# Kernel optimization log

Hardware: AMD Instinct MI355X
Metric: run time of the kernel (lower is better)

## Reference

```python
import jax, jax.numpy as jnp
import numpy as np

N_GRAPHS = 64

def setup_inputs() -> dict:
    key = jax.random.key(0)
    ks = jax.random.split(key, 8)
    N, E, H = 50000, 600000, 128
    x = jax.random.normal(ks[0], (N, 2), dtype=jnp.float32)
    edge_index = jax.random.randint(ks[1], (2, E), 0, N, dtype=jnp.int64)
    batch = jnp.sort(jax.random.randint(ks[2], (N,), 0, N_GRAPHS, dtype=jnp.int64))
    s = 0.1  # keep tanh out of saturation
    return {
        'x': x,
        'edge_index': edge_index,
        'batch': batch,
        'W1': jax.random.normal(ks[3], (2, H), dtype=jnp.float32) * s,
        'b1': jnp.zeros((H,), jnp.float32),
        'W2': jax.random.normal(ks[4], (H, H), dtype=jnp.float32) * s,
        'b2': jnp.zeros((H,), jnp.float32),
        'W3': jax.random.normal(ks[5], (H, H), dtype=jnp.float32) * s,
        'b3': jnp.zeros((H,), jnp.float32),
        'Wo': jax.random.normal(ks[6], (2 * H, 41), dtype=jnp.float32) * s,
        'bo': jnp.zeros((41,), jnp.float32),
    }

def reference(x, edge_index, batch, W1, b1, W2, b2, W3, b3, Wo, bo):
    N = x.shape[0]
    src, dst = edge_index[0], edge_index[1]
    # GCN symmetric normalization with self loops: deg = in-degree + 1
    ones_e = jnp.ones(src.shape[0], dtype=x.dtype)
    deg = jax.ops.segment_sum(ones_e, dst, num_segments=N) + 1.0
    dinv = jax.lax.rsqrt(deg)                       # [N]
    edge_norm = (dinv[src] * dinv[dst])[:, None]    # [E,1]
    self_norm = (dinv * dinv)[:, None]              # [N,1]

    def gcn(h, W, b):
        h = h @ W                                   # [N,H] transform first
        agg = jax.ops.segment_sum(h[src] * edge_norm, dst, num_segments=N)
        return agg + h * self_norm + b

    h = jnp.tanh(gcn(x, W1, b1))
    h = jnp.tanh(gcn(h, W2, b2))
    h = jnp.tanh(gcn(h, W3, b3))

    # global max pool + global mean pool over graphs
    cnt = jax.ops.segment_sum(jnp.ones(N, dtype=h.dtype), batch, num_segments=N_GRAPHS)
    mx = jax.ops.segment_max(h, batch, num_segments=N_GRAPHS)
    mx = jnp.where(cnt[:, None] > 0, mx, 0.0)
    mean = jax.ops.segment_sum(h, batch, num_segments=N_GRAPHS) / jnp.maximum(cnt, 1.0)[:, None]
    pooled = jnp.concatenate([mx, mean], axis=1)    # [G, 2H]
    return jnp.tanh(pooled @ Wo + bo)               # [G, 41]
```

## Files before the change

### kernel.cpp

```cpp
#include <hip/hip_runtime.h>
#include <math.h>

#define NGRAPH 64
#define POOL_CHUNKS 32
#define SCAN_BLK 1024

typedef short short8 __attribute__((ext_vector_type(8)));
typedef float floatx4 __attribute__((ext_vector_type(4)));

__device__ inline unsigned pack_bf16x2(float a, float b) {
    unsigned ua = __float_as_uint(a);
    unsigned ub = __float_as_uint(b);
    ua = (ua + 0x7fffu + ((ua >> 16) & 1u)) >> 16;
    ub = (ub + 0x7fffu + ((ub >> 16) & 1u)) >> 16;
    return ua | (ub << 16);
}
__device__ inline unsigned short bf16_1(float a) {
    unsigned ua = __float_as_uint(a);
    return (unsigned short)((ua + 0x7fffu + ((ua >> 16) & 1u)) >> 16);
}
__device__ inline float bf16lo(unsigned u) { return __uint_as_float(u << 16); }
__device__ inline float bf16hi(unsigned u) { return __uint_as_float(u & 0xffff0000u); }


__global__ void pack_count(const int* __restrict__ dst, int E, int* __restrict__ cnt,
                           const float* __restrict__ W2, const float* __restrict__ W3,
                           unsigned* __restrict__ Wt2, unsigned* __restrict__ Wt3) {
    if (blockIdx.x < 32) {
        int b = blockIdx.x;
        const float* W = (b < 16) ? W2 : W3;
        unsigned* Wt = (b < 16) ? Wt2 : Wt3;
        b &= 15;
        int bk = b & 3, bn = b >> 2;
        __shared__ float s[32][33];
        int tx = threadIdx.x & 31, ty = threadIdx.x >> 5;
#pragma unroll
        for (int r = 0; r < 4; ++r)
            s[r * 8 + ty][tx] = W[(bk * 32 + r * 8 + ty) * 128 + bn * 32 + tx];
        __syncthreads();
        int t16 = threadIdx.x & 15, tn = threadIdx.x >> 4;
#pragma unroll
        for (int pass = 0; pass < 2; ++pass) {
            int nl = pass * 16 + tn;
            unsigned pk = pack_bf16x2(s[2 * t16][nl], s[2 * t16 + 1][nl]);
            Wt[(bn * 32 + nl) * 64 + bk * 16 + t16] = pk;
        }
    } else {
        int e = (blockIdx.x - 32) * blockDim.x + threadIdx.x;
        if (e < E) atomicAdd(&cnt[dst[e]], 1);
    }
}


__global__ __launch_bounds__(SCAN_BLK) void scan_phase1(const int* __restrict__ cnt,
                                                        const float* __restrict__ x,
                                                        int* __restrict__ row_ptr,
                                                        int* __restrict__ bsum,
                                                        float* __restrict__ dinv,
                                                        float2* __restrict__ y, int N) {
    __shared__ int sm[SCAN_BLK];
    int i = blockIdx.x * SCAN_BLK + threadIdx.x;
    int v = (i < N) ? cnt[i] : 0;
    if (i < N) {
        float dv = rsqrtf((float)v + 1.0f);
        dinv[i] = dv;
        float2 xv = ((const float2*)x)[i];
        y[i] = make_float2(xv.x * dv, xv.y * dv);
    }
    sm[threadIdx.x] = v;
    __syncthreads();
    for (int off = 1; off < SCAN_BLK; off <<= 1) {
        int t = (threadIdx.x >= (unsigned)off) ? sm[threadIdx.x - off] : 0;
        __syncthreads();
        sm[threadIdx.x] += t;
        __syncthreads();
    }
    if (i < N) row_ptr[i] = sm[threadIdx.x] - v;
    if (threadIdx.x == SCAN_BLK - 1) bsum[blockIdx.x] = sm[SCAN_BLK - 1];
}

__global__ __launch_bounds__(SCAN_BLK) void scan_phase2(int* __restrict__ bsum, int nb,
                                                        const int* __restrict__ batch, int N,
                                                        int* __restrict__ goff) {
    if (threadIdx.x <= NGRAPH) {
        int g = threadIdx.x;
        int lo = 0, hi = N;
        while (lo < hi) {
            int mid = (lo + hi) >> 1;
            if (batch[mid] < g) lo = mid + 1; else hi = mid;
        }
        goff[g] = lo;
    }
    __shared__ int sm[SCAN_BLK];
    int v = (threadIdx.x < (unsigned)nb) ? bsum[threadIdx.x] : 0;
    sm[threadIdx.x] = v;
    __syncthreads();
    for (int off = 1; off < SCAN_BLK; off <<= 1) {
        int t = (threadIdx.x >= (unsigned)off) ? sm[threadIdx.x - off] : 0;
        __syncthreads();
        sm[threadIdx.x] += t;
        __syncthreads();
    }
    if (threadIdx.x < (unsigned)nb) bsum[threadIdx.x] = sm[threadIdx.x] - v;
}

__global__ __launch_bounds__(SCAN_BLK) void scan_phase3(int* __restrict__ row_ptr,
                                                        const int* __restrict__ bsum,
                                                        int N, int E) {
    int i = blockIdx.x * SCAN_BLK + threadIdx.x;
    if (i < N) row_ptr[i] += bsum[blockIdx.x];
    if (i == 0) row_ptr[N] = E;
}

__global__ void fill_kernel(const int* __restrict__ src, const int* __restrict__ dst, int E,
                            const int* __restrict__ row_ptr, int* __restrict__ cnt,
                            int* __restrict__ col) {
    int e = blockIdx.x * blockDim.x + threadIdx.x;
    if (e < E) {
        int d = dst[e];
        int p = row_ptr[d] + atomicSub(&cnt[d], 1) - 1;
        col[p] = src[e];
    }
}


__global__ __launch_bounds__(256) void agg_x_t1(const float2* __restrict__ y,
                                                const int* __restrict__ row_ptr,
                                                const int* __restrict__ col,
                                                const float* __restrict__ dinv,
                                                const float* __restrict__ W1,
                                                const float* __restrict__ b1,
                                                unsigned short* __restrict__ h, int N) {
    __shared__ float4 sW[64];
    __shared__ float4 sb[32];
    __shared__ float2 zs[256];
    if (threadIdx.x < 64) sW[threadIdx.x] = ((const float4*)W1)[threadIdx.x];
    if (threadIdx.x < 32) sb[threadIdx.x] = ((const float4*)b1)[threadIdx.x];

    int v = blockIdx.x * 256 + threadIdx.x;
    float2 zv = make_float2(0.f, 0.f);
    if (v < N) {
        int s = row_ptr[v], e = row_ptr[v + 1];
        float2 a0 = y[v];
        float2 a1 = make_float2(0.f, 0.f);
        float2 a2 = make_float2(0.f, 0.f);
        float2 a3 = make_float2(0.f, 0.f);
        int j = s;
        for (; j + 4 <= e; j += 4) {
            int u0 = col[j], u1 = col[j + 1], u2 = col[j + 2], u3 = col[j + 3];
            float2 v0 = y[u0], v1 = y[u1], v2 = y[u2], v3 = y[u3];
            a0.x += v0.x; a0.y += v0.y;
            a1.x += v1.x; a1.y += v1.y;
            a2.x += v2.x; a2.y += v2.y;
            a3.x += v3.x; a3.y += v3.y;
        }
        for (; j < e; ++j) {
            float2 vv = y[col[j]];
            a0.x += vv.x; a0.y += vv.y;
        }
        float dv = dinv[v];
        zv = make_float2(dv * (a0.x + a1.x + a2.x + a3.x),
                         dv * (a0.y + a1.y + a2.y + a3.y));
    }
    zs[threadIdx.x] = zv;
    __syncthreads();

    int q = threadIdx.x & 31;
    int rsub = threadIdx.x >> 5;
    float4 w0 = sW[q];
    float4 w1 = sW[32 + q];
    float4 b = sb[q];
#pragma unroll 4
    for (int pass = 0; pass < 32; ++pass) {
        int local = pass * 8 + rsub;
        int row = blockIdx.x * 256 + local;
        if (row >= N) break;
        float2 z = zs[local];
        float ox = tanhf(fmaf(z.x, w0.x, fmaf(z.y, w1.x, b.x)));
        float oy = tanhf(fmaf(z.x, w0.y, fmaf(z.y, w1.y, b.y)));
        float oz = tanhf(fmaf(z.x, w0.z, fmaf(z.y, w1.z, b.z)));
        float ow = tanhf(fmaf(z.x, w0.w, fmaf(z.y, w1.w, b.w)));
        uint2 pk;
        pk.x = pack_bf16x2(ox, oy);
        pk.y = pack_bf16x2(oz, ow);
        ((uint2*)h)[(size_t)row * 32 + q] = pk;
    }
}


__global__ __launch_bounds__(256) void gemm_mfma(const unsigned short* __restrict__ A,
                                                 const unsigned* __restrict__ Wt,
                                                 const float* __restrict__ dinv,
                                                 unsigned short* __restrict__ t, int N) {
    __shared__ unsigned sW[128 * 68];
    const uint4* Wt4 = (const uint4*)Wt;
    for (int i = threadIdx.x; i < 2048; i += 256) {
        int n = i >> 4, c = i & 15;
        *(uint4*)&sW[n * 68 + c * 4] = Wt4[i];
    }
    __syncthreads();
    int w = threadIdx.x >> 6;
    int l = threadIdx.x & 63;
    int lm = l & 15;
    int q4 = l >> 4;
    int k8 = q4 * 8;

    floatx4 acc[2][8];
#pragma unroll
    for (int i = 0; i < 2; ++i)
#pragma unroll
        for (int j = 0; j < 8; ++j) acc[i][j] = (floatx4){0.f, 0.f, 0.f, 0.f};

    int rowbase = blockIdx.x * 128 + w * 32;
#pragma unroll
    for (int ks = 0; ks < 4; ++ks) {
        int k0 = ks * 32 + k8;
        short8 a[2];
#pragma unroll
        for (int mt = 0; mt < 2; ++mt) {
            int r = min(rowbase + mt * 16 + lm, N - 1);
            a[mt] = *(const short8*)(A + (size_t)r * 128 + k0);
        }
#pragma unroll
        for (int nt = 0; nt < 8; ++nt) {
            short8 b = *(const short8*)&sW[(nt * 16 + lm) * 68 + ks * 16 + q4 * 4];
#pragma unroll
            for (int mt = 0; mt < 2; ++mt)
                acc[mt][nt] = __builtin_amdgcn_mfma_f32_16x16x32_bf16(a[mt], b, acc[mt][nt], 0, 0, 0);
        }
    }

#pragma unroll
    for (int mt = 0; mt < 2; ++mt) {
#pragma unroll
        for (int reg = 0; reg < 4; ++reg) {
            int gr = rowbase + mt * 16 + q4 * 4 + reg;
            if (gr >= N) continue;
            float dv = dinv[gr];
#pragma unroll
            for (int nt = 0; nt < 8; ++nt) {
                int c = nt * 16 + lm;
                t[(size_t)gr * 128 + c] = bf16_1(acc[mt][nt][reg] * dv);
            }
        }
    }
}


__global__ __launch_bounds__(256) void agg_kernel(const unsigned short* __restrict__ t,
                                                  const int* __restrict__ row_ptr,
                                                  const int* __restrict__ col,
                                                  const float* __restrict__ dinv,
                                                  const float* __restrict__ bias,
                                                  unsigned short* __restrict__ out, int N) {
    int wave = threadIdx.x >> 6;
    int lane = threadIdx.x & 63;
    int i = lane >> 4;
    int q = lane & 15;
    int node = blockIdx.x * 4 + wave;
    if (node >= N) return;
    int s = row_ptr[node];
    int deg = row_ptr[node + 1] - s;
    const uint4* t4 = (const uint4*)t;

    float a0[8], a1[8];
#pragma unroll
    for (int k = 0; k < 8; ++k) { a0[k] = 0.f; a1[k] = 0.f; }
    if (i == 0) {
        uint4 v = t4[(size_t)node * 16 + q];
        a0[0] = bf16lo(v.x); a0[1] = bf16hi(v.x);
        a0[2] = bf16lo(v.y); a0[3] = bf16hi(v.y);
        a0[4] = bf16lo(v.z); a0[5] = bf16hi(v.z);
        a0[6] = bf16lo(v.w); a0[7] = bf16hi(v.w);
    }
    int j = 0;
    for (; j + 8 <= deg; j += 8) {
        int u0 = col[s + j + i];
        int u1 = col[s + j + 4 + i];
        uint4 v0 = t4[(size_t)u0 * 16 + q];
        uint4 v1 = t4[(size_t)u1 * 16 + q];
        a0[0] += bf16lo(v0.x); a0[1] += bf16hi(v0.x);
        a0[2] += bf16lo(v0.y); a0[3] += bf16hi(v0.y);
        a0[4] += bf16lo(v0.z); a0[5] += bf16hi(v0.z);
        a0[6] += bf16lo(v0.w); a0[7] += bf16hi(v0.w);
        a1[0] += bf16lo(v1.x); a1[1] += bf16hi(v1.x);
        a1[2] += bf16lo(v1.y); a1[3] += bf16hi(v1.y);
        a1[4] += bf16lo(v1.z); a1[5] += bf16hi(v1.z);
        a1[6] += bf16lo(v1.w); a1[7] += bf16hi(v1.w);
    }
    for (; j < deg; j += 4) {
        if (j + i < deg) {
            int u = col[s + j + i];
            uint4 v = t4[(size_t)u * 16 + q];
            a0[0] += bf16lo(v.x); a0[1] += bf16hi(v.x);
            a0[2] += bf16lo(v.y); a0[3] += bf16hi(v.y);
            a0[4] += bf16lo(v.z); a0[5] += bf16hi(v.z);
            a0[6] += bf16lo(v.w); a0[7] += bf16hi(v.w);
        }
    }
#pragma unroll
    for (int k = 0; k < 8; ++k) {
        float v = a0[k] + a1[k];
        v += __shfl_xor(v, 16, 64);
        v += __shfl_xor(v, 32, 64);
        a0[k] = v;
    }
    if (i == 0) {
        float dv = dinv[node];
        float4 b0 = ((const float4*)bias)[2 * q];
        float4 b1 = ((const float4*)bias)[2 * q + 1];
        uint4 pk;
        pk.x = pack_bf16x2(tanhf(fmaf(dv, a0[0], b0.x)), tanhf(fmaf(dv, a0[1], b0.y)));
        pk.y = pack_bf16x2(tanhf(fmaf(dv, a0[2], b0.z)), tanhf(fmaf(dv, a0[3], b0.w)));
        pk.z = pack_bf16x2(tanhf(fmaf(dv, a0[4], b1.x)), tanhf(fmaf(dv, a0[5], b1.y)));
        pk.w = pack_bf16x2(tanhf(fmaf(dv, a0[6], b1.z)), tanhf(fmaf(dv, a0[7], b1.w)));
        ((uint4*)out)[(size_t)node * 16 + q] = pk;
    }
}


__global__ __launch_bounds__(128) void pool_partial(const unsigned short* __restrict__ h,
                                                    const int* __restrict__ goff,
                                                    float* __restrict__ part) {
    int g = blockIdx.x;
    int c = blockIdx.y;
    int j = threadIdx.x;
    int s = goff[g], e = goff[g + 1];
    int cnt = e - s;
    int per = (cnt + POOL_CHUNKS - 1) / POOL_CHUNKS;
    int ps = s + c * per;
    int pe = min(ps + per, e);
    float mx = -3.402823466e+38f, sm = 0.f;
    for (int n = ps; n < pe; ++n) {
        float v = __uint_as_float(((unsigned)h[(size_t)n * 128 + j]) << 16);
        mx = fmaxf(mx, v);
        sm += v;
    }
    float* dst = part + ((size_t)g * POOL_CHUNKS + c) * 256;
    dst[j] = mx;
    dst[128 + j] = sm;
}

__global__ __launch_bounds__(128) void pool_final(const float* __restrict__ part,
                                                  const int* __restrict__ goff,
                                                  const float* __restrict__ Wo,
                                                  const float* __restrict__ bo,
                                                  float* __restrict__ out) {
    __shared__ float p[256];
    int g = blockIdx.x;
    int j = threadIdx.x;
    float mx = -3.402823466e+38f, sm = 0.f;
    const float* base = part + (size_t)g * POOL_CHUNKS * 256;
#pragma unroll 4
    for (int c = 0; c < POOL_CHUNKS; ++c) {
        mx = fmaxf(mx, base[c * 256 + j]);
        sm += base[c * 256 + 128 + j];
    }
    int cnt = goff[g + 1] - goff[g];
    p[j] = (cnt > 0) ? mx : 0.f;
    p[128 + j] = sm / fmaxf((float)cnt, 1.f);
    __syncthreads();
    if (j < 41) {
        float acc = bo[j];
        for (int k = 0; k < 256; ++k) acc = fmaf(p[k], Wo[k * 41 + j], acc);
        out[g * 41 + j] = tanhf(acc);
    }
}


extern "C" void kernel_launch(void* const* d_in, const int* in_sizes, int n_in,
                              void* d_out, int out_size, void* d_ws, size_t ws_size,
                              hipStream_t stream) {
    const float* x   = (const float*)d_in[0];
    const int*   ei  = (const int*)d_in[1];
    const int* batch = (const int*)d_in[2];
    const float* W1  = (const float*)d_in[3];
    const float* b1  = (const float*)d_in[4];
    const float* W2  = (const float*)d_in[5];
    const float* b2  = (const float*)d_in[6];
    const float* W3  = (const float*)d_in[7];
    const float* b3  = (const float*)d_in[8];
    const float* Wo  = (const float*)d_in[9];
    const float* bo  = (const float*)d_in[10];
    float* outp = (float*)d_out;

    int N = in_sizes[2];
    int E = in_sizes[1] / 2;
    const int* src = ei;
    const int* dst = ei + E;

    char* p = (char*)d_ws;
    auto alloc = [&](size_t bytes) -> char* {
        char* q = p;
        p += (bytes + 255) & ~(size_t)255;
        return q;
    };
    unsigned short* t   = (unsigned short*)alloc((size_t)N * 128 * 2);
    unsigned short* hb  = (unsigned short*)alloc((size_t)N * 128 * 2);
    unsigned short* h3b = (unsigned short*)alloc((size_t)N * 128 * 2);
    float* dinv   = (float*)alloc((size_t)N * 4);
    int*   cnt    = (int*)alloc((size_t)N * 4);
    int*   rowp   = (int*)alloc((size_t)(N + 1) * 4);
    int*   col    = (int*)alloc((size_t)E * 4);
    int*   goff   = (int*)alloc(65 * 4);
    float* part   = (float*)alloc((size_t)NGRAPH * POOL_CHUNKS * 256 * 4);
    float2* y     = (float2*)alloc((size_t)N * 8);
    unsigned* Wt2 = (unsigned*)alloc(128 * 64 * 4);
    unsigned* Wt3 = (unsigned*)alloc(128 * 64 * 4);
    int nscan = (N + SCAN_BLK - 1) / SCAN_BLK;
    int*   bsum   = (int*)alloc((size_t)nscan * 4);

    hipMemsetAsync(cnt, 0, (size_t)N * 4, stream);

    pack_count<<<32 + (E + 255) / 256, 256, 0, stream>>>(dst, E, cnt, W2, W3, Wt2, Wt3);
    scan_phase1<<<nscan, SCAN_BLK, 0, stream>>>(cnt, x, rowp, bsum, dinv, y, N);
    scan_phase2<<<1, SCAN_BLK, 0, stream>>>(bsum, nscan, batch, N, goff);
    scan_phase3<<<nscan, SCAN_BLK, 0, stream>>>(rowp, bsum, N, E);
    fill_kernel<<<(E + 255) / 256, 256, 0, stream>>>(src, dst, E, rowp, cnt, col);

    agg_x_t1<<<(N + 255) / 256, 256, 0, stream>>>(y, rowp, col, dinv, W1, b1, hb, N);
    gemm_mfma<<<(N + 127) / 128, 256, 0, stream>>>(hb, Wt2, dinv, t, N);
    agg_kernel<<<(N + 3) / 4, 256, 0, stream>>>(t, rowp, col, dinv, b2, hb, N);
    gemm_mfma<<<(N + 127) / 128, 256, 0, stream>>>(hb, Wt3, dinv, t, N);
    agg_kernel<<<(N + 3) / 4, 256, 0, stream>>>(t, rowp, col, dinv, b3, h3b, N);

    dim3 pgrid(NGRAPH, POOL_CHUNKS);
    pool_partial<<<pgrid, 128, 0, stream>>>(h3b, goff, part);
    pool_final<<<NGRAPH, 128, 0, stream>>>(part, goff, Wo, bo, outp);
}
```

Measured before the change: 276.4 us.

## Split node features into four 32-column slabs and aggregate per slab

Node feature buffers move from row-major [N,128] to four column slabs of [N,32], and every producer and consumer (agg_x_t1, gemm_mfma, agg_kernel, pool_partial) is rewritten for the new layout. The aggregation kernel gains a second grid dimension over slabs, and each wave now gathers 16 neighbours at a time, 64 bytes per neighbour. The aim is a smaller working set per gather pass so the gathered feature slab stays in L2/LLC. The cost is four times as many aggregation blocks, re-reading the CSR indices once per slab, and narrower 64-byte gathers.

```diff
diff --git a/kernel.cpp b/kernel.cpp
--- a/kernel.cpp
+++ b/kernel.cpp
@@ -21,6 +21,7 @@
 }
 __device__ inline float bf16lo(unsigned u) { return __uint_as_float(u << 16); }
 __device__ inline float bf16hi(unsigned u) { return __uint_as_float(u & 0xffff0000u); }
+
 
 
 __global__ void pack_count(const int* __restrict__ dst, int E, int* __restrict__ cnt,
@@ -170,6 +171,7 @@
     float4 w0 = sW[q];
     float4 w1 = sW[32 + q];
     float4 b = sb[q];
+    size_t qoff = (size_t)(q >> 3) * N;
 #pragma unroll 4
     for (int pass = 0; pass < 32; ++pass) {
         int local = pass * 8 + rsub;
@@ -183,7 +185,7 @@
         uint2 pk;
         pk.x = pack_bf16x2(ox, oy);
         pk.y = pack_bf16x2(oz, ow);
-        ((uint2*)h)[(size_t)row * 32 + q] = pk;
+        ((uint2*)h)[(qoff + row) * 8 + (q & 7)] = pk;
     }
 }
 
@@ -214,12 +216,11 @@
     int rowbase = blockIdx.x * 128 + w * 32;
 #pragma unroll
     for (int ks = 0; ks < 4; ++ks) {
-        int k0 = ks * 32 + k8;
         short8 a[2];
 #pragma unroll
         for (int mt = 0; mt < 2; ++mt) {
             int r = min(rowbase + mt * 16 + lm, N - 1);
-            a[mt] = *(const short8*)(A + (size_t)r * 128 + k0);
+            a[mt] = *(const short8*)(A + ((size_t)ks * N + r) * 32 + k8);
         }
 #pragma unroll
         for (int nt = 0; nt < 8; ++nt) {
@@ -239,8 +240,8 @@
             float dv = dinv[gr];
 #pragma unroll
             for (int nt = 0; nt < 8; ++nt) {
-                int c = nt * 16 + lm;
-                t[(size_t)gr * 128 + c] = bf16_1(acc[mt][nt][reg] * dv);
+                t[((size_t)(nt >> 1) * N + gr) * 32 + (nt & 1) * 16 + lm] =
+                    bf16_1(acc[mt][nt][reg] * dv);
             }
         }
     }
@@ -255,73 +256,69 @@
                                                   unsigned short* __restrict__ out, int N) {
     int wave = threadIdx.x >> 6;
     int lane = threadIdx.x & 63;
-    int i = lane >> 4;
-    int q = lane & 15;
+    int i = lane >> 2;
+    int q = lane & 3;
+    int qt = blockIdx.y;
     int node = blockIdx.x * 4 + wave;
     if (node >= N) return;
     int s = row_ptr[node];
     int deg = row_ptr[node + 1] - s;
     const uint4* t4 = (const uint4*)t;
-
-    float a0[8], a1[8];
-#pragma unroll
-    for (int k = 0; k < 8; ++k) { a0[k] = 0.f; a1[k] = 0.f; }
+    size_t qbase = (size_t)qt * N;
+
+    float a[8];
+#pragma unroll
+    for (int k = 0; k < 8; ++k) a[k] = 0.f;
     if (i == 0) {
-        uint4 v = t4[(size_t)node * 16 + q];
-        a0[0] = bf16lo(v.x); a0[1] = bf16hi(v.x);
-        a0[2] = bf16lo(v.y); a0[3] = bf16hi(v.y);
-        a0[4] = bf16lo(v.z); a0[5] = bf16hi(v.z);
-        a0[6] = bf16lo(v.w); a0[7] = bf16hi(v.w);
+        uint4 v = t4[(qbase + node) * 4 + q];
+        a[0] = bf16lo(v.x); a[1] = bf16hi(v.x);
+        a[2] = bf16lo(v.y); a[3] = bf16hi(v.y);
+        a[4] = bf16lo(v.z); a[5] = bf16hi(v.z);
+        a[6] = bf16lo(v.w); a[7] = bf16hi(v.w);
     }
     int j = 0;
-    for (; j + 8 <= deg; j += 8) {
-        int u0 = col[s + j + i];
-        int u1 = col[s + j + 4 + i];
-        uint4 v0 = t4[(size_t)u0 * 16 + q];
-        uint4 v1 = t4[(size_t)u1 * 16 + q];
-        a0[0] += bf16lo(v0.x); a0[1] += bf16hi(v0.x);
-        a0[2] += bf16lo(v0.y); a0[3] += bf16hi(v0.y);
-        a0[4] += bf16lo(v0.z); a0[5] += bf16hi(v0.z);
-        a0[6] += bf16lo(v0.w); a0[7] += bf16hi(v0.w);
-        a1[0] += bf16lo(v1.x); a1[1] += bf16hi(v1.x);
-        a1[2] += bf16lo(v1.y); a1[3] += bf16hi(v1.y);
-        a1[4] += bf16lo(v1.z); a1[5] += bf16hi(v1.z);
-        a1[6] += bf16lo(v1.w); a1[7] += bf16hi(v1.w);
-    }
-    for (; j < deg; j += 4) {
-        if (j + i < deg) {
-            int u = col[s + j + i];
-            uint4 v = t4[(size_t)u * 16 + q];
-            a0[0] += bf16lo(v.x); a0[1] += bf16hi(v.x);
-            a0[2] += bf16lo(v.y); a0[3] += bf16hi(v.y);
-            a0[4] += bf16lo(v.z); a0[5] += bf16hi(v.z);
-            a0[6] += bf16lo(v.w); a0[7] += bf16hi(v.w);
-        }
+    for (; j + 16 <= deg; j += 16) {
+        int u = col[s + j + i];
+        uint4 v = t4[(qbase + u) * 4 + q];
+        a[0] += bf16lo(v.x); a[1] += bf16hi(v.x);
+        a[2] += bf16lo(v.y); a[3] += bf16hi(v.y);
+        a[4] += bf16lo(v.z); a[5] += bf16hi(v.z);
+        a[6] += bf16lo(v.w); a[7] += bf16hi(v.w);
+    }
+    if (j + i < deg) {
+        int u = col[s + j + i];
+        uint4 v = t4[(qbase + u) * 4 + q];
+        a[0] += bf16lo(v.x); a[1] += bf16hi(v.x);
+        a[2] += bf16lo(v.y); a[3] += bf16hi(v.y);
+        a[4] += bf16lo(v.z); a[5] += bf16hi(v.z);
+        a[6] += bf16lo(v.w); a[7] += bf16hi(v.w);
     }
 #pragma unroll
     for (int k = 0; k < 8; ++k) {
-        float v = a0[k] + a1[k];
+        float v = a[k];
+        v += __shfl_xor(v, 4, 64);
+        v += __shfl_xor(v, 8, 64);
         v += __shfl_xor(v, 16, 64);
         v += __shfl_xor(v, 32, 64);
-        a0[k] = v;
+        a[k] = v;
     }
     if (i == 0) {
         float dv = dinv[node];
-        float4 b0 = ((const float4*)bias)[2 * q];
-        float4 b1 = ((const float4*)bias)[2 * q + 1];
+        float4 b0 = ((const float4*)bias)[qt * 8 + q * 2];
+        float4 b1 = ((const float4*)bias)[qt * 8 + q * 2 + 1];
         uint4 pk;
-        pk.x = pack_bf16x2(tanhf(fmaf(dv, a0[0], b0.x)), tanhf(fmaf(dv, a0[1], b0.y)));
-        pk.y = pack_bf16x2(tanhf(fmaf(dv, a0[2], b0.z)), tanhf(fmaf(dv, a0[3], b0.w)));
-        pk.z = pack_bf16x2(tanhf(fmaf(dv, a0[4], b1.x)), tanhf(fmaf(dv, a0[5], b1.y)));
-        pk.w = pack_bf16x2(tanhf(fmaf(dv, a0[6], b1.z)), tanhf(fmaf(dv, a0[7], b1.w)));
-        ((uint4*)out)[(size_t)node * 16 + q] = pk;
+        pk.x = pack_bf16x2(tanhf(fmaf(dv, a[0], b0.x)), tanhf(fmaf(dv, a[1], b0.y)));
+        pk.y = pack_bf16x2(tanhf(fmaf(dv, a[2], b0.z)), tanhf(fmaf(dv, a[3], b0.w)));
+        pk.z = pack_bf16x2(tanhf(fmaf(dv, a[4], b1.x)), tanhf(fmaf(dv, a[5], b1.y)));
+        pk.w = pack_bf16x2(tanhf(fmaf(dv, a[6], b1.z)), tanhf(fmaf(dv, a[7], b1.w)));
+        ((uint4*)out)[(qbase + node) * 4 + q] = pk;
     }
 }
 
 
 __global__ __launch_bounds__(128) void pool_partial(const unsigned short* __restrict__ h,
                                                     const int* __restrict__ goff,
-                                                    float* __restrict__ part) {
+                                                    float* __restrict__ part, int N) {
     int g = blockIdx.x;
     int c = blockIdx.y;
     int j = threadIdx.x;
@@ -330,9 +327,11 @@
     int per = (cnt + POOL_CHUNKS - 1) / POOL_CHUNKS;
     int ps = s + c * per;
     int pe = min(ps + per, e);
+    size_t qoff = (size_t)(j >> 5) * N;
+    int jq = j & 31;
     float mx = -3.402823466e+38f, sm = 0.f;
     for (int n = ps; n < pe; ++n) {
-        float v = __uint_as_float(((unsigned)h[(size_t)n * 128 + j]) << 16);
+        float v = __uint_as_float(((unsigned)h[(qoff + n) * 32 + jq]) << 16);
         mx = fmaxf(mx, v);
         sm += v;
     }
@@ -418,13 +417,15 @@
     scan_phase3<<<nscan, SCAN_BLK, 0, stream>>>(rowp, bsum, N, E);
     fill_kernel<<<(E + 255) / 256, 256, 0, stream>>>(src, dst, E, rowp, cnt, col);
 
+    dim3 agrid((N + 3) / 4, 4);
+
     agg_x_t1<<<(N + 255) / 256, 256, 0, stream>>>(y, rowp, col, dinv, W1, b1, hb, N);
     gemm_mfma<<<(N + 127) / 128, 256, 0, stream>>>(hb, Wt2, dinv, t, N);
-    agg_kernel<<<(N + 3) / 4, 256, 0, stream>>>(t, rowp, col, dinv, b2, hb, N);
+    agg_kernel<<<agrid, 256, 0, stream>>>(t, rowp, col, dinv, b2, hb, N);
     gemm_mfma<<<(N + 127) / 128, 256, 0, stream>>>(hb, Wt3, dinv, t, N);
-    agg_kernel<<<(N + 3) / 4, 256, 0, stream>>>(t, rowp, col, dinv, b3, h3b, N);
+    agg_kernel<<<agrid, 256, 0, stream>>>(t, rowp, col, dinv, b3, h3b, N);
 
     dim3 pgrid(NGRAPH, POOL_CHUNKS);
-    pool_partial<<<pgrid, 128, 0, stream>>>(h3b, goff, part);
+    pool_partial<<<pgrid, 128, 0, stream>>>(h3b, goff, part, N);
     pool_final<<<NGRAPH, 128, 0, stream>>>(part, goff, Wo, bo, outp);
 }
```

Result: slower. 363.8 us (+31.6%).
